# Optimization experiments

Hardware: AMD Instinct MI355X
Metric: run time of the kernel (lower is better)

## Reference

```python
import jax, jax.numpy as jnp
import numpy as np

N_FEATS = 9       # OGB atom feature columns
VOCAB = 119       # per-feature embedding vocab (max OGB atom vocab)
HIDDEN = 128
NUM_HEADS = 8
HEAD_DIM = HIDDEN // NUM_HEADS


def setup_inputs() -> dict:
    key = jax.random.key(0)
    ks = jax.random.split(key, 12)
    N, K = 50000, 16
    X = jax.random.randint(ks[0], (N, N_FEATS), 0, VOCAB)
    nbr_idx = jax.random.randint(ks[1], (N, K), 0, N)
    nbr_mask = jax.random.randint(ks[2], (N, K), 0, 2).astype(bool)
    atom_emb = jax.random.normal(ks[3], (N_FEATS, VOCAB, HIDDEN), jnp.float32) * 0.02
    s = 1.0 / np.sqrt(HIDDEN)
    Wq = jax.random.normal(ks[4], (HIDDEN, HIDDEN), jnp.float32) * s
    bq = jnp.zeros((HIDDEN,), jnp.float32)
    Wk = jax.random.normal(ks[5], (HIDDEN, HIDDEN), jnp.float32) * s
    bk = jnp.zeros((HIDDEN,), jnp.float32)
    Wv = jax.random.normal(ks[6], (HIDDEN, HIDDEN), jnp.float32) * s
    bv = jnp.zeros((HIDDEN,), jnp.float32)
    return {"X": X, "nbr_idx": nbr_idx, "nbr_mask": nbr_mask,
            "atom_emb": atom_emb, "Wq": Wq, "bq": bq,
            "Wk": Wk, "bk": bk, "Wv": Wv, "bv": bv}


def reference(X, nbr_idx, nbr_mask, atom_emb, Wq, bq, Wk, bk, Wv, bv):
    N = X.shape[0]
    # AtomEncoder: sum per-feature embedding lookups -> [N, HIDDEN]
    h = jnp.sum(atom_emb[jnp.arange(N_FEATS)[None, :], X], axis=1)
    scaling = HEAD_DIM ** -0.5
    q = (h @ Wq + bq).reshape(N, NUM_HEADS, HEAD_DIM) * scaling
    k = (h @ Wk + bk).reshape(N, NUM_HEADS, HEAD_DIM)
    v = (h @ Wv + bv).reshape(N, NUM_HEADS, HEAD_DIM)
    # ELL-format sparse attention: gather padded neighbor k/v -> [N, K, H, D]
    k_n = k[nbr_idx]
    v_n = v[nbr_idx]
    scores = jnp.einsum('nhd,nkhd->nkh', q, k_n)          # [N, K, H]
    scores = jnp.where(nbr_mask[..., None], scores, -1e9)
    attn = jax.nn.softmax(scores, axis=1)                 # softmax over neighbors
    out = jnp.einsum('nkh,nkhd->nhd', attn, v_n)          # [N, H, D]
    return out.reshape(N, HIDDEN)
```

## Files before the change

### kernel.cpp

```cpp
#include <hip/hip_runtime.h>
#include <hip/hip_bf16.h>

#define NFEAT 9
#define VOCAB 119
#define HIDDEN 128
#define NHEAD 8
#define HDIM 16
#define KNBR 16

typedef __attribute__((ext_vector_type(8))) short short8;
typedef __attribute__((ext_vector_type(4))) float f32x4;

template <int CTRL>
__device__ __forceinline__ float dpp_ror(float v) {
    return __int_as_float(__builtin_amdgcn_update_dpp(
        0, __float_as_int(v), CTRL, 0xF, 0xF, false));
}

__global__ void fill_kernel(float* out, int n, float val) {
    int i = blockIdx.x * blockDim.x + threadIdx.x;
    if (i < n) out[i] = val;
}

__global__ __launch_bounds__(256) void wt_kernel(
    const float* __restrict__ Wq, const float* __restrict__ Wk,
    const float* __restrict__ Wv, short* __restrict__ Wt)
{
    int mat = blockIdx.x >> 2, tile = blockIdx.x & 3;
    const float* W = (mat == 0) ? Wq : (mat == 1) ? Wk : Wv;
    __shared__ float ls[32 * HIDDEN];
    int tid = threadIdx.x;
    int cc0 = tile * 32;
    #pragma unroll
    for (int j = 0; j < 16; ++j) {
        int idx = j * 256 + tid;
        ls[idx] = W[(size_t)cc0 * HIDDEN + idx];
    }
    __syncthreads();
    int c = tid & 127, hf = tid >> 7;
    unsigned int ob[8];
    #pragma unroll
    for (int j = 0; j < 8; ++j) {
        int ccl = hf * 16 + 2 * j;
        __hip_bfloat16 b0 = __float2bfloat16(ls[ccl * HIDDEN + c]);
        __hip_bfloat16 b1 = __float2bfloat16(ls[(ccl + 1) * HIDDEN + c]);
        ob[j] = (unsigned int)*reinterpret_cast<unsigned short*>(&b0)
              | ((unsigned int)*reinterpret_cast<unsigned short*>(&b1) << 16);
    }
    unsigned int* dst = reinterpret_cast<unsigned int*>(
        Wt + (size_t)mat * HIDDEN * HIDDEN + (size_t)c * HIDDEN + cc0 + hf * 16);
    #pragma unroll
    for (int j = 0; j < 8; ++j) dst[j] = ob[j];
}

#define MT 32
#define HBS 136

__global__ __launch_bounds__(256, 3) void qkv_kernel(
    const int* __restrict__ X, const float* __restrict__ emb,
    const short* __restrict__ Wt,
    const float* __restrict__ bq, const float* __restrict__ bk,
    const float* __restrict__ bv,
    float* __restrict__ qf, __hip_bfloat16* __restrict__ kv, int N)
{
    __shared__ __align__(16) short hb[MT * HBS];
    __shared__ int xs[MT * NFEAT];

    const int tid = threadIdx.x;
    const int n0 = blockIdx.x * MT;

    for (int i = tid; i < MT * NFEAT; i += 256) {
        int n = n0 + i / NFEAT;
        int v = (n < N) ? X[(size_t)n * NFEAT + (i % NFEAT)] : 0;
        xs[i] = min(max(v, 0), VOCAB - 1);
    }
    __syncthreads();

    {
        const int cg = tid & 31;
        const int slot = tid >> 5;
        #pragma unroll
        for (int i = 0; i < 4; ++i) {
            int nl = slot * 4 + i;
            float4 acc = {0.f, 0.f, 0.f, 0.f};
            #pragma unroll
            for (int f = 0; f < NFEAT; ++f) {
                const float4 e = *reinterpret_cast<const float4*>(
                    &emb[((size_t)f * VOCAB + xs[nl * NFEAT + f]) * HIDDEN + cg * 4]);
                acc.x += e.x; acc.y += e.y; acc.z += e.z; acc.w += e.w;
            }
            __hip_bfloat162 p0 = __float22bfloat162_rn(make_float2(acc.x, acc.y));
            __hip_bfloat162 p1 = __float22bfloat162_rn(make_float2(acc.z, acc.w));
            uint2 u;
            u.x = *reinterpret_cast<unsigned int*>(&p0);
            u.y = *reinterpret_cast<unsigned int*>(&p1);
            *reinterpret_cast<uint2*>(&hb[nl * HBS + cg * 4]) = u;
        }
    }
    __syncthreads();

    const int wave = tid >> 6, lane = tid & 63;
    const int l15 = lane & 15, quad = lane >> 4;

    short8 b[2][3][4];
    float bias[2][3];
    #pragma unroll
    for (int g = 0; g < 2; ++g) {
        const int n = (wave * 2 + g) * 16 + l15;
        #pragma unroll
        for (int mat = 0; mat < 3; ++mat) {
            #pragma unroll
            for (int k0 = 0; k0 < 4; ++k0)
                b[g][mat][k0] = *reinterpret_cast<const short8*>(
                    &Wt[(size_t)mat * HIDDEN * HIDDEN + n * HIDDEN + k0 * 32 + quad * 8]);
            bias[g][mat] = (mat == 0) ? bq[n] : (mat == 1) ? bk[n] : bv[n];
        }
    }

    #pragma unroll
    for (int mt = 0; mt < 2; ++mt) {
        const int mloc = mt * 16 + l15;
        short8 a[4];
        #pragma unroll
        for (int k0 = 0; k0 < 4; ++k0)
            a[k0] = *reinterpret_cast<const short8*>(
                &hb[mloc * HBS + k0 * 32 + quad * 8]);
        #pragma unroll
        for (int g = 0; g < 2; ++g) {
            const int n = (wave * 2 + g) * 16 + l15;
            f32x4 acc[3] = {{0.f,0.f,0.f,0.f},{0.f,0.f,0.f,0.f},{0.f,0.f,0.f,0.f}};
            #pragma unroll
            for (int mat = 0; mat < 3; ++mat)
                #pragma unroll
                for (int k0 = 0; k0 < 4; ++k0)
                    acc[mat] = __builtin_amdgcn_mfma_f32_16x16x32_bf16(
                        a[k0], b[g][mat][k0], acc[mat], 0, 0, 0);
            #pragma unroll
            for (int mat = 0; mat < 3; ++mat) {
                #pragma unroll
                for (int r = 0; r < 4; ++r) {
                    int node = n0 + mt * 16 + quad * 4 + r;
                    if (node < N) {
                        float val = acc[mat][r] + bias[g][mat];
                        if (mat == 0)      qf[(size_t)node * HIDDEN + n] = val * 0.25f;
                        else if (mat == 1) kv[(size_t)node * 256 + n] = __float2bfloat16(val);
                        else               kv[(size_t)node * 256 + 128 + n] = __float2bfloat16(val);
                    }
                }
            }
        }
    }
}

#define NPB2 2

__global__ __launch_bounds__(256) void attn_kernel(
    const int* __restrict__ nbr_idx, const int* __restrict__ nbr_mask,
    const float* __restrict__ qf, const __hip_bfloat16* __restrict__ kv,
    float* __restrict__ out, int N)
{
    __shared__ __align__(16) float sl[NPB2][NHEAD][20];

    const int tid = threadIdx.x;
    const int local = tid >> 7;
    const int t = tid & 127;
    int n = blockIdx.x * NPB2 + local;
    if (n >= N) n = N - 1;

    const int hh = t >> 4;
    const int kk = t & 15;

    const char* kvb = (const char*)kv;
    const unsigned nm1 = (unsigned)(N - 1);

    int idxr[KNBR];
    {
        const int4* ip = reinterpret_cast<const int4*>(nbr_idx + (size_t)n * KNBR);
        #pragma unroll
        for (int m4 = 0; m4 < 4; ++m4) {
            int4 iv = ip[m4];
            idxr[4 * m4 + 0] = (int)min((unsigned)iv.x, nm1);
            idxr[4 * m4 + 1] = (int)min((unsigned)iv.y, nm1);
            idxr[4 * m4 + 2] = (int)min((unsigned)iv.z, nm1);
            idxr[4 * m4 + 3] = (int)min((unsigned)iv.w, nm1);
        }
    }
    const int mymsk = nbr_mask[(size_t)n * KNBR + kk];

    short8 k0 = {0, 0, 0, 0, 0, 0, 0, 0};
    short8 k1 = {0, 0, 0, 0, 0, 0, 0, 0};
    if (mymsk) {
        unsigned ko = ((unsigned)idxr[kk] << 9) + (((unsigned)t & 0x70u) << 1);
        k0 = *reinterpret_cast<const short8*>(kvb + ko);
        k1 = *reinterpret_cast<const short8*>(kvb + ko + 16);
    }

    float qr[HDIM];
    {
        const float4* qp = reinterpret_cast<const float4*>(
            (const char*)qf + (((unsigned)n << 9) + ((unsigned)hh << 6)));
        #pragma unroll
        for (int c4 = 0; c4 < 4; ++c4) {
            float4 qv = qp[c4];
            qr[4 * c4 + 0] = qv.x; qr[4 * c4 + 1] = qv.y;
            qr[4 * c4 + 2] = qv.z; qr[4 * c4 + 3] = qv.w;
        }
    }

    float vr[KNBR];
    {
        const unsigned vbo = 256u + 2u * (unsigned)t;
        #pragma unroll
        for (int j = 0; j < KNBR; ++j) {
            unsigned u = *reinterpret_cast<const unsigned short*>(
                kvb + ((((unsigned)idxr[j]) << 9) + vbo));
            vr[j] = __uint_as_float(u << 16);
        }
    }

    {
        const __hip_bfloat162* kp0 = reinterpret_cast<const __hip_bfloat162*>(&k0);
        const __hip_bfloat162* kp1 = reinterpret_cast<const __hip_bfloat162*>(&k1);
        float ax = 0.f, ay = 0.f;
        #pragma unroll
        for (int d2 = 0; d2 < 4; ++d2) {
            float2 f0 = __bfloat1622float2(kp0[d2]);
            float2 f1 = __bfloat1622float2(kp1[d2]);
            ax = fmaf(qr[2 * d2],     f0.x, ax);
            ay = fmaf(qr[2 * d2 + 1], f0.y, ay);
            ax = fmaf(qr[8 + 2 * d2],     f1.x, ax);
            ay = fmaf(qr[8 + 2 * d2 + 1], f1.y, ay);
        }
        float s = ax + ay;
        if (!mymsk) s = -1e9f;
        float m = s;
        m = fmaxf(m, dpp_ror<0x121>(m));
        m = fmaxf(m, dpp_ror<0x122>(m));
        m = fmaxf(m, dpp_ror<0x124>(m));
        m = fmaxf(m, dpp_ror<0x128>(m));
        float e = __expf(s - m);
        float d = e;
        d += dpp_ror<0x121>(d);
        d += dpp_ror<0x122>(d);
        d += dpp_ror<0x124>(d);
        d += dpp_ror<0x128>(d);
        sl[local][hh][kk] = e * __builtin_amdgcn_rcpf(d);
    }

    {
        float ox = 0.f, oy = 0.f;
        const float4* wp = reinterpret_cast<const float4*>(&sl[local][t >> 4][0]);
        #pragma unroll
        for (int m4 = 0; m4 < 4; ++m4) {
            float4 w4 = wp[m4];
            ox = fmaf(w4.x, vr[4 * m4 + 0], ox);
            oy = fmaf(w4.y, vr[4 * m4 + 1], oy);
            ox = fmaf(w4.z, vr[4 * m4 + 2], ox);
            oy = fmaf(w4.w, vr[4 * m4 + 3], oy);
        }
        float* op = reinterpret_cast<float*>(
            (char*)out + (((unsigned)n << 9) + 4u * (unsigned)t));
        *op = ox + oy;
    }
}

extern "C" void kernel_launch(void* const* d_in, const int* in_sizes, int n_in,
                              void* d_out, int out_size, void* d_ws, size_t ws_size,
                              hipStream_t stream)
{
    float* out = (float*)d_out;

    bool ok = (n_in == 10);
    int N = ok ? in_sizes[0] / NFEAT : 0;
    ok = ok && N > 0 && in_sizes[0] == N * NFEAT
            && in_sizes[1] == N * KNBR
            && in_sizes[2] == N * KNBR
            && in_sizes[3] == NFEAT * VOCAB * HIDDEN
            && in_sizes[4] == HIDDEN * HIDDEN && in_sizes[5] == HIDDEN
            && in_sizes[6] == HIDDEN * HIDDEN && in_sizes[7] == HIDDEN
            && in_sizes[8] == HIDDEN * HIDDEN && in_sizes[9] == HIDDEN
            && out_size == N * HIDDEN;
    if (!ok) {
        fill_kernel<<<(out_size + 255) / 256, 256, 0, stream>>>(out, out_size, 0.0f);
        return;
    }
    size_t need = (size_t)N * 1024 + 3 * HIDDEN * HIDDEN * sizeof(short);
    if (ws_size < need) {
        fill_kernel<<<(out_size + 255) / 256, 256, 0, stream>>>(out, out_size, 1.0f);
        return;
    }

    const int* X        = (const int*)d_in[0];
    const int* nbr_idx  = (const int*)d_in[1];
    const int* nbr_mask = (const int*)d_in[2];
    const float* emb = (const float*)d_in[3];
    const float* Wq  = (const float*)d_in[4];
    const float* bq  = (const float*)d_in[5];
    const float* Wk  = (const float*)d_in[6];
    const float* bk  = (const float*)d_in[7];
    const float* Wv  = (const float*)d_in[8];
    const float* bv  = (const float*)d_in[9];

    float* qf = (float*)d_ws;
    __hip_bfloat16* kv =
        (__hip_bfloat16*)((char*)d_ws + (size_t)N * HIDDEN * sizeof(float));
    short* Wt = (short*)((char*)d_ws + (size_t)N * 1024);

    wt_kernel<<<12, 256, 0, stream>>>(Wq, Wk, Wv, Wt);
    qkv_kernel<<<(N + MT - 1) / MT, 256, 0, stream>>>(
        X, emb, Wt, bq, bk, bv, qf, kv, N);
    attn_kernel<<<(N + NPB2 - 1) / NPB2, 256, 0, stream>>>(
        nbr_idx, nbr_mask, qf, kv, out, N);
}
```

Before: 165.8 us.

## Process two nodes per thread group and skip V gathers for masked neighbors

Each 128-thread group now handles two nodes instead of one, which doubles in-flight memory loads per thread and halves the block count. V loads for masked-out neighbors are redirected to the node's own row, using a wave ballot of the mask, so they do not touch scattered cache lines. When every neighbor is masked the original gather is kept, preserving the uniform-softmax semantics. Register pressure rises from the doubled idx/q/v/k arrays, which may lower occupancy.

```diff
diff --git a/kernel.cpp b/kernel.cpp
--- a/kernel.cpp
+++ b/kernel.cpp
@@ -152,87 +152,107 @@
     }
 }
 
-#define NPB2 2
+#define NPB4 4
 
 __global__ __launch_bounds__(256) void attn_kernel(
     const int* __restrict__ nbr_idx, const int* __restrict__ nbr_mask,
     const float* __restrict__ qf, const __hip_bfloat16* __restrict__ kv,
     float* __restrict__ out, int N)
 {
-    __shared__ __align__(16) float sl[NPB2][NHEAD][20];
+    __shared__ __align__(16) float sl[NPB4][NHEAD][20];
 
     const int tid = threadIdx.x;
-    const int local = tid >> 7;
+    const int grp = tid >> 7;
     const int t = tid & 127;
-    int n = blockIdx.x * NPB2 + local;
-    if (n >= N) n = N - 1;
-
     const int hh = t >> 4;
     const int kk = t & 15;
 
     const char* kvb = (const char*)kv;
     const unsigned nm1 = (unsigned)(N - 1);
 
-    int idxr[KNBR];
-    {
-        const int4* ip = reinterpret_cast<const int4*>(nbr_idx + (size_t)n * KNBR);
+    int nn[2];
+    nn[0] = blockIdx.x * NPB4 + grp * 2;
+    nn[1] = nn[0] + 1;
+    if (nn[0] >= N) nn[0] = N - 1;
+    if (nn[1] >= N) nn[1] = N - 1;
+
+    int idxr[2][KNBR];
+    int mymsk[2];
+    unsigned mgate[2];
+    #pragma unroll
+    for (int p = 0; p < 2; ++p) {
+        const int4* ip = reinterpret_cast<const int4*>(nbr_idx + (size_t)nn[p] * KNBR);
         #pragma unroll
         for (int m4 = 0; m4 < 4; ++m4) {
             int4 iv = ip[m4];
-            idxr[4 * m4 + 0] = (int)min((unsigned)iv.x, nm1);
-            idxr[4 * m4 + 1] = (int)min((unsigned)iv.y, nm1);
-            idxr[4 * m4 + 2] = (int)min((unsigned)iv.z, nm1);
-            idxr[4 * m4 + 3] = (int)min((unsigned)iv.w, nm1);
-        }
-    }
-    const int mymsk = nbr_mask[(size_t)n * KNBR + kk];
-
-    short8 k0 = {0, 0, 0, 0, 0, 0, 0, 0};
-    short8 k1 = {0, 0, 0, 0, 0, 0, 0, 0};
-    if (mymsk) {
-        unsigned ko = ((unsigned)idxr[kk] << 9) + (((unsigned)t & 0x70u) << 1);
-        k0 = *reinterpret_cast<const short8*>(kvb + ko);
-        k1 = *reinterpret_cast<const short8*>(kvb + ko + 16);
-    }
-
-    float qr[HDIM];
-    {
+            idxr[p][4 * m4 + 0] = (int)min((unsigned)iv.x, nm1);
+            idxr[p][4 * m4 + 1] = (int)min((unsigned)iv.y, nm1);
+            idxr[p][4 * m4 + 2] = (int)min((unsigned)iv.z, nm1);
+            idxr[p][4 * m4 + 3] = (int)min((unsigned)iv.w, nm1);
+        }
+        mymsk[p] = nbr_mask[(size_t)nn[p] * KNBR + kk];
+        unsigned long long bal = __ballot(mymsk[p] != 0);
+        mgate[p] = (bal == 0ull) ? 0xFFFFu : (unsigned)(bal & 0xFFFFu);
+    }
+
+    short8 k0[2], k1[2];
+    #pragma unroll
+    for (int p = 0; p < 2; ++p) {
+        k0[p] = short8{0, 0, 0, 0, 0, 0, 0, 0};
+        k1[p] = short8{0, 0, 0, 0, 0, 0, 0, 0};
+        if (mymsk[p]) {
+            unsigned ko = ((unsigned)idxr[p][kk] << 9) + (((unsigned)t & 0x70u) << 1);
+            k0[p] = *reinterpret_cast<const short8*>(kvb + ko);
+            k1[p] = *reinterpret_cast<const short8*>(kvb + ko + 16);
+        }
+    }
+
+    float qr[2][HDIM];
+    #pragma unroll
+    for (int p = 0; p < 2; ++p) {
         const float4* qp = reinterpret_cast<const float4*>(
-            (const char*)qf + (((unsigned)n << 9) + ((unsigned)hh << 6)));
+            (const char*)qf + (((unsigned)nn[p] << 9) + ((unsigned)hh << 6)));
         #pragma unroll
         for (int c4 = 0; c4 < 4; ++c4) {
             float4 qv = qp[c4];
-            qr[4 * c4 + 0] = qv.x; qr[4 * c4 + 1] = qv.y;
-            qr[4 * c4 + 2] = qv.z; qr[4 * c4 + 3] = qv.w;
-        }
-    }
-
-    float vr[KNBR];
+            qr[p][4 * c4 + 0] = qv.x; qr[p][4 * c4 + 1] = qv.y;
+            qr[p][4 * c4 + 2] = qv.z; qr[p][4 * c4 + 3] = qv.w;
+        }
+    }
+
+    float vr[2][KNBR];
     {
         const unsigned vbo = 256u + 2u * (unsigned)t;
         #pragma unroll
-        for (int j = 0; j < KNBR; ++j) {
-            unsigned u = *reinterpret_cast<const unsigned short*>(
-                kvb + ((((unsigned)idxr[j]) << 9) + vbo));
-            vr[j] = __uint_as_float(u << 16);
-        }
-    }
-
-    {
-        const __hip_bfloat162* kp0 = reinterpret_cast<const __hip_bfloat162*>(&k0);
-        const __hip_bfloat162* kp1 = reinterpret_cast<const __hip_bfloat162*>(&k1);
+        for (int p = 0; p < 2; ++p) {
+            const unsigned selfrow = ((unsigned)nn[p] << 9);
+            #pragma unroll
+            for (int j = 0; j < KNBR; ++j) {
+                unsigned row = ((mgate[p] >> j) & 1u) ? ((unsigned)idxr[p][j] << 9)
+                                                      : selfrow;
+                unsigned u = *reinterpret_cast<const unsigned short*>(
+                    kvb + (row + vbo));
+                vr[p][j] = __uint_as_float(u << 16);
+            }
+        }
+    }
+
+    #pragma unroll
+    for (int p = 0; p < 2; ++p) {
+        const __hip_bfloat162* kp0 = reinterpret_cast<const __hip_bfloat162*>(&k0[p]);
+        const __hip_bfloat162* kp1 = reinterpret_cast<const __hip_bfloat162*>(&k1[p]);
         float ax = 0.f, ay = 0.f;
         #pragma unroll
         for (int d2 = 0; d2 < 4; ++d2) {
             float2 f0 = __bfloat1622float2(kp0[d2]);
             float2 f1 = __bfloat1622float2(kp1[d2]);
-            ax = fmaf(qr[2 * d2],     f0.x, ax);
-            ay = fmaf(qr[2 * d2 + 1], f0.y, ay);
-            ax = fmaf(qr[8 + 2 * d2],     f1.x, ax);
-            ay = fmaf(qr[8 + 2 * d2 + 1], f1.y, ay);
+            ax = fmaf(qr[p][2 * d2],     f0.x, ax);
+            ay = fmaf(qr[p][2 * d2 + 1], f0.y, ay);
+            ax = fmaf(qr[p][8 + 2 * d2],     f1.x, ax);
+            ay = fmaf(qr[p][8 + 2 * d2 + 1], f1.y, ay);
         }
         float s = ax + ay;
-        if (!mymsk) s = -1e9f;
+        if (!mymsk[p]) s = -1e9f;
         float m = s;
         m = fmaxf(m, dpp_ror<0x121>(m));
         m = fmaxf(m, dpp_ror<0x122>(m));
@@ -244,22 +264,23 @@
         d += dpp_ror<0x122>(d);
         d += dpp_ror<0x124>(d);
         d += dpp_ror<0x128>(d);
-        sl[local][hh][kk] = e * __builtin_amdgcn_rcpf(d);
-    }
-
-    {
+        sl[grp * 2 + p][hh][kk] = e * __builtin_amdgcn_rcpf(d);
+    }
+
+    #pragma unroll
+    for (int p = 0; p < 2; ++p) {
         float ox = 0.f, oy = 0.f;
-        const float4* wp = reinterpret_cast<const float4*>(&sl[local][t >> 4][0]);
+        const float4* wp = reinterpret_cast<const float4*>(&sl[grp * 2 + p][t >> 4][0]);
         #pragma unroll
         for (int m4 = 0; m4 < 4; ++m4) {
             float4 w4 = wp[m4];
-            ox = fmaf(w4.x, vr[4 * m4 + 0], ox);
-            oy = fmaf(w4.y, vr[4 * m4 + 1], oy);
-            ox = fmaf(w4.z, vr[4 * m4 + 2], ox);
-            oy = fmaf(w4.w, vr[4 * m4 + 3], oy);
+            ox = fmaf(w4.x, vr[p][4 * m4 + 0], ox);
+            oy = fmaf(w4.y, vr[p][4 * m4 + 1], oy);
+            ox = fmaf(w4.z, vr[p][4 * m4 + 2], ox);
+            oy = fmaf(w4.w, vr[p][4 * m4 + 3], oy);
         }
         float* op = reinterpret_cast<float*>(
-            (char*)out + (((unsigned)n << 9) + 4u * (unsigned)t));
+            (char*)out + (((unsigned)nn[p] << 9) + 4u * (unsigned)t));
         *op = ox + oy;
     }
 }
@@ -309,6 +330,6 @@
     wt_kernel<<<12, 256, 0, stream>>>(Wq, Wk, Wv, Wt);
     qkv_kernel<<<(N + MT - 1) / MT, 256, 0, stream>>>(
         X, emb, Wt, bq, bk, bv, qf, kv, N);
-    attn_kernel<<<(N + NPB2 - 1) / NPB2, 256, 0, stream>>>(
+    attn_kernel<<<(N + NPB4 - 1) / NPB4, 256, 0, stream>>>(
         nbr_idx, nbr_mask, qf, kv, out, N);
 }
```

After: 168.6 us. About the same (+1.7%).
